# Performance work log

Measured on AMD Instinct MI355X. Metric: run time of the kernel, lower is better.

The kernel has to match this reference:

```python
import jax, jax.numpy as jnp
import numpy as np

H, W = 32, 56
CK, CV = 64, 512
N = 16 * H * W  # long + work memory fully populated: 16 frames of H*W entries
TOP_K = 30


def setup_inputs() -> dict:
    key = jax.random.key(0)
    k1, k2, k3, k4, k5 = jax.random.split(key, 5)
    return {
        "q_key": jax.random.normal(k1, (1, CK, H, W), dtype=jnp.float32),
        "q_selection": jax.random.uniform(k2, (1, CK, H, W), dtype=jnp.float32),
        "mem_key": jax.random.normal(k3, (1, CK, N), dtype=jnp.float32),
        "mem_shrinkage": jax.random.uniform(k4, (1, N, 1), dtype=jnp.float32),
        "mem_value": jax.random.normal(k5, (2, CV, N), dtype=jnp.float32),
    }


def reference(q_key, q_selection, mem_key, mem_shrinkage, mem_value):
    b, ck, h, w = q_key.shape
    hw = h * w
    qk = q_key.reshape(1, ck, hw)          # [1, CK, HW]
    qs = q_selection.reshape(1, ck, hw)    # [1, CK, HW]

    mk = jnp.swapaxes(mem_key, 1, 2)       # [1, N, CK]
    # negative weighted squared L2 distance via matmul algebra
    a_sq = jnp.matmul(mk * mk, qs)                    # [1, N, HW]
    two_ab = 2.0 * jnp.matmul(mk, qk * qs)            # [1, N, HW]
    b_sq = jnp.sum(qs * qk * qk, axis=1, keepdims=True)  # [1, 1, HW]
    sim = (-a_sq + two_ab - b_sq) * mem_shrinkage / jnp.sqrt(jnp.float32(ck))  # [1, N, HW]

    # topk over the memory axis (dim=1), softmax over selected entries, scatter back
    simT = jnp.swapaxes(sim, 1, 2)                    # [1, HW, N]
    vals, idx = jax.lax.top_k(simT, TOP_K)            # [1, HW, K]
    x_exp = jnp.exp(vals)
    x_exp = x_exp / jnp.sum(x_exp, axis=-1, keepdims=True)
    i0 = jnp.arange(1)[:, None, None]
    i1 = jnp.arange(hw)[None, :, None]
    affT = jnp.zeros_like(simT).at[i0, i1, idx].set(x_exp)  # [1, HW, N]
    affinity = jnp.swapaxes(affT, 1, 2)               # [1, N, HW]

    out = jnp.matmul(mem_value, affinity)             # [2, CV, HW] (batch-broadcast)
    return out.reshape(2, CV, h, w)
```

## Files before the change

### kernel.cpp

```cpp
#include <hip/hip_runtime.h>
#include <math.h>

#define HW      1792
#define NMEM    28672
#define NCHUNK  3584
#define TOPK    30
#define CTARGET 64
#define SCAP    80
#define SIMB    448
#define WPS     7

typedef __attribute__((ext_vector_type(8))) short bf16x8;
typedef __attribute__((ext_vector_type(8))) unsigned short u16x8;
typedef __attribute__((ext_vector_type(4))) float f32x4;
typedef __attribute__((ext_vector_type(4))) _Float16 h4;

static __device__ __forceinline__ unsigned short f2bf(float v) {
  unsigned b = __float_as_uint(v);
  return (unsigned short)((b + 0x7FFFu + ((b >> 16) & 1u)) >> 16);
}
static __device__ __forceinline__ float bf2f(unsigned short h) {
  return __uint_as_float(((unsigned)h) << 16);
}
static __device__ __forceinline__ unsigned fkey(float v) {
  return __float_as_uint(-v) & 0x7FFFFFFFu;
}
static __device__ __forceinline__ void gl_lds16(const void* g, void* l) {
  __builtin_amdgcn_global_load_lds(
      (const __attribute__((address_space(1))) unsigned*)g,
      (__attribute__((address_space(3))) unsigned*)l, 16, 0, 0);
}
#define WSYNC() do { asm volatile("s_waitcnt lgkmcnt(0)" ::: "memory"); \
                     __builtin_amdgcn_wave_barrier(); } while (0)

__global__ __launch_bounds__(256)
void k_prep_b(const float* __restrict__ mk, const float* __restrict__ shr_in,
              unsigned short* __restrict__ Bh,
              float* __restrict__ mkT, float* __restrict__ shr_s)
{
  const int n = blockIdx.x * 256 + threadIdx.x;
  shr_s[n] = shr_in[n] * 0.125f;
  for (int cb = 0; cb < 64; cb += 8) {
    u16x8 h1, h2;
    float vv[8];
    #pragma unroll
    for (int j = 0; j < 8; ++j) {
      float v = mk[(size_t)(cb + j) * NMEM + n];
      vv[j] = v;
      h1[j] = f2bf(v);
      h2[j] = f2bf(v * v);
    }
    const int s = cb >> 3;
    *reinterpret_cast<u16x8*>(&Bh[((size_t)s * NMEM + n) * 8])       = h1;
    *reinterpret_cast<u16x8*>(&Bh[((size_t)(s + 8) * NMEM + n) * 8]) = h2;
    *reinterpret_cast<float4*>(&mkT[(size_t)n * 64 + cb])     = make_float4(vv[0], vv[1], vv[2], vv[3]);
    *reinterpret_cast<float4*>(&mkT[(size_t)n * 64 + cb + 4]) = make_float4(vv[4], vv[5], vv[6], vv[7]);
  }
}

__global__ __launch_bounds__(256)
void k_prep_u(const float* __restrict__ q_key, const float* __restrict__ q_sel,
              unsigned short* __restrict__ Uh, unsigned short* __restrict__ Ul,
              float* __restrict__ bsq)
{
  const int p = blockIdx.x * 256 + threadIdx.x;
  float bs = 0.f;
  for (int cb = 0; cb < 64; cb += 8) {
    u16x8 h1, l1, h2, l2;
    #pragma unroll
    for (int j = 0; j < 8; ++j) {
      int c = cb + j;
      float k = q_key[(size_t)c * HW + p];
      float s = q_sel[(size_t)c * HW + p];
      float u = 2.f * k * s;
      float w = -s;
      bs = fmaf(s * k, k, bs);
      unsigned short h = f2bf(u); h1[j] = h; l1[j] = f2bf(u - bf2f(h));
      unsigned short g = f2bf(w); h2[j] = g; l2[j] = f2bf(w - bf2f(g));
    }
    const int s = cb >> 3;
    *reinterpret_cast<u16x8*>(&Uh[((size_t)s * HW + p) * 8])       = h1;
    *reinterpret_cast<u16x8*>(&Ul[((size_t)s * HW + p) * 8])       = l1;
    *reinterpret_cast<u16x8*>(&Uh[((size_t)(s + 8) * HW + p) * 8]) = h2;
    *reinterpret_cast<u16x8*>(&Ul[((size_t)(s + 8) * HW + p) * 8]) = l2;
  }
  bsq[p] = bs;
}

__global__ __launch_bounds__(256, 2)
void k_sim(const unsigned short* __restrict__ Uh, const unsigned short* __restrict__ Ul,
           const unsigned short* __restrict__ Bh,
           const float* __restrict__ bsq, const float* __restrict__ shr_s,
           float* __restrict__ pmax)
{
  __shared__ char smem[65536] __attribute__((aligned(16)));
  const int tid = threadIdx.x;
  const int wid = tid >> 6, lane = tid & 63;
  const int lr = lane & 15, lg = lane >> 4;
  const int pb = blockIdx.x % 14, st = blockIdx.x / 14;
  const int pw = pb * 128 + wid * 32;
  const int w0 = st * WPS;

  bf16x8 a0h[4], a0l[4], a1h[4], a1l[4];
  #pragma unroll
  for (int t = 0; t < 4; ++t) {
    const size_t e0 = ((size_t)(t * 4 + lg) * HW + pw + lr) * 8;
    const size_t e1 = e0 + 16 * 8;
    a0h[t] = *reinterpret_cast<const bf16x8*>(&Uh[e0]);
    a0l[t] = *reinterpret_cast<const bf16x8*>(&Ul[e0]);
    a1h[t] = *reinterpret_cast<const bf16x8*>(&Uh[e1]);
    a1l[t] = *reinterpret_cast<const bf16x8*>(&Ul[e1]);
  }
  float bq[2][4];
  #pragma unroll
  for (int pt = 0; pt < 2; ++pt)
    #pragma unroll
    for (int r = 0; r < 4; ++r) bq[pt][r] = bsq[pw + pt * 16 + 4 * lg + r];

  auto stage = [&](int buf, int i) {
    const int n0 = (w0 + i) * 128;
    #pragma unroll
    for (int j = 0; j < 8; ++j) {
      const int idx = j * 256 + tid;
      const int s = idx >> 7, rr = idx & 127;
      gl_lds16((const char*)Bh + ((size_t)s * NMEM + n0 + rr) * 16,
               smem + buf * 32768 + idx * 16);
    }
  };

  stage(0, 0);
  int buf = 0;
  for (int i = 0; i < WPS; ++i) {
    __syncthreads();
    if (i + 1 < WPS) stage(buf ^ 1, i + 1);

    f32x4 acc[2][8];
    #pragma unroll
    for (int a = 0; a < 2; ++a)
      #pragma unroll
      for (int b = 0; b < 8; ++b) acc[a][b] = (f32x4){0.f, 0.f, 0.f, 0.f};

    const short* lb = (const short*)(smem + buf * 32768);
    #pragma unroll
    for (int t = 0; t < 4; ++t) {
      #pragma unroll
      for (int nt = 0; nt < 8; ++nt) {
        bf16x8 bh = *reinterpret_cast<const bf16x8*>(
            &lb[((t * 4 + lg) * 128 + nt * 16 + lr) * 8]);
        acc[0][nt] = __builtin_amdgcn_mfma_f32_16x16x32_bf16(a0h[t], bh, acc[0][nt], 0, 0, 0);
        acc[0][nt] = __builtin_amdgcn_mfma_f32_16x16x32_bf16(a0l[t], bh, acc[0][nt], 0, 0, 0);
        acc[1][nt] = __builtin_amdgcn_mfma_f32_16x16x32_bf16(a1h[t], bh, acc[1][nt], 0, 0, 0);
        acc[1][nt] = __builtin_amdgcn_mfma_f32_16x16x32_bf16(a1l[t], bh, acc[1][nt], 0, 0, 0);
      }
    }

    const int wgl = w0 + i;
    const int n0 = wgl * 128;
    float shv[8];
    #pragma unroll
    for (int nt = 0; nt < 8; ++nt) shv[nt] = shr_s[n0 + nt * 16 + lr];
    #pragma unroll
    for (int pt = 0; pt < 2; ++pt) {
      #pragma unroll
      for (int r = 0; r < 4; ++r) {
        float mx = -INFINITY;
        #pragma unroll
        for (int nt = 0; nt < 8; ++nt)
          mx = fmaxf(mx, (acc[pt][nt][r] - bq[pt][r]) * shv[nt]);
        pmax[(size_t)(pw + pt * 16 + 4 * lg + r) * NCHUNK + wgl * 16 + lr] = mx;
      }
    }
    buf ^= 1;
  }
}

__device__ __forceinline__ void wave_cross(const int* h, int lane, int target,
                                           int& B, int& nA)
{
  int hv[16]; int ls = 0;
  #pragma unroll
  for (int k = 0; k < 16; ++k) { hv[k] = h[(k << 6) + lane]; ls += hv[k]; }
  int sc = ls;
  #pragma unroll
  for (int off = 1; off < 64; off <<= 1) {
    int t = __shfl_up(sc, off);
    if (lane >= off) sc += t;
  }
  int run = sc - ls;
  int myB = -1, mynA = 0;
  #pragma unroll
  for (int k = 0; k < 16; ++k) {
    if (run < target && run + hv[k] >= target) { myB = lane * 16 + k; mynA = run; }
    run += hv[k];
  }
  unsigned long long ball = __ballot(myB >= 0);
  int src = __ffsll((long long)ball) - 1;
  B = __shfl(myB, src); nA = __shfl(mynA, src);
}

__global__ __launch_bounds__(256, 2)
void k_select(const float* __restrict__ pmax, const float* __restrict__ mkT,
              const float* __restrict__ q_key, const float* __restrict__ q_sel,
              const float* __restrict__ shr_s,
              float* __restrict__ wgt, int* __restrict__ widx)
{
  __shared__ int                hist[4][1024];
  __shared__ unsigned long long pk[4][640];
  __shared__ short              slist[4][SCAP];
  __shared__ float              sqk[4][64], sqs[4][64];

  const int w = threadIdx.x >> 6, lane = threadIdx.x & 63;
  const int pix = blockIdx.x * 4 + w;
  int* h = hist[w];
  unsigned long long* p = pk[w];
  short* sl = slist[w];

  auto ph = [](int b) { return ((b & 15) << 6) | (b >> 4); };

  sqk[w][lane] = q_key[(size_t)lane * HW + pix];
  sqs[w][lane] = q_sel[(size_t)lane * HW + pix];

  float m[56];
  const float* pm = pmax + (size_t)pix * NCHUNK;
  #pragma unroll
  for (int j = 0; j < 56; ++j) m[j] = pm[lane + 64 * j];

  #pragma unroll
  for (int k = 0; k < 16; ++k) h[lane + 64 * k] = 0;
  WSYNC();
  #pragma unroll
  for (int j = 0; j < 56; ++j) atomicAdd(&h[ph(fkey(m[j]) >> 21)], 1);
  WSYNC();
  int B1, nA1;
  wave_cross(h, lane, CTARGET, B1, nA1);

  #pragma unroll
  for (int k = 0; k < 16; ++k) h[lane + 64 * k] = 0;
  WSYNC();
  #pragma unroll
  for (int j = 0; j < 56; ++j) {
    unsigned u = fkey(m[j]);
    if ((int)(u >> 21) == B1) atomicAdd(&h[ph((u >> 11) & 1023)], 1);
  }
  WSYNC();
  int Bs1, nAs1;
  wave_cross(h, lane, CTARGET - nA1, Bs1, nAs1);

  int nsurv = 0;
  #pragma unroll
  for (int j = 0; j < 56; ++j) {
    unsigned u = fkey(m[j]);
    int bin = (int)(u >> 21);
    bool keep = (bin < B1) || (bin == B1 && (int)((u >> 11) & 1023) <= Bs1);
    unsigned long long ball = __ballot(keep);
    if (keep) {
      int pos = nsurv + __popcll(ball & ((1ull << lane) - 1ull));
      if (pos < SCAP) sl[pos] = (short)(lane + 64 * j);
    }
    nsurv += __popcll(ball);
  }
  nsurv = (nsurv < SCAP) ? nsurv : SCAP;
  const int NC = nsurv * 8;

  #pragma unroll
  for (int t = 0; t < 10; ++t) p[lane + (t << 6)] = 0ull;
  WSYNC();
  const float4* k4p = reinterpret_cast<const float4*>(sqk[w]);
  const float4* s4p = reinterpret_cast<const float4*>(sqs[w]);
  for (int c = lane; c < NC; c += 64) {
    const int cc = sl[c >> 3];
    const int n = ((cc >> 4) << 7) + (cc & 15) + ((c & 7) << 4);
    const float4* mr = reinterpret_cast<const float4*>(mkT + (size_t)n * 64);
    float a0 = 0.f, a1 = 0.f, a2 = 0.f, a3 = 0.f;
    #pragma unroll
    for (int j = 0; j < 16; j += 4) {
      #pragma unroll
      for (int jj = 0; jj < 4; ++jj) {
        float4 q = mr[j + jj], kk = k4p[j + jj], ss = s4p[j + jj];
        float d0 = q.x - kk.x, d1 = q.y - kk.y, d2 = q.z - kk.z, d3 = q.w - kk.w;
        float pj = fmaf(ss.x * d0, d0,
                   fmaf(ss.y * d1, d1,
                   fmaf(ss.z * d2, d2, ss.w * d3 * d3)));
        if (jj == 0) a0 += pj; else if (jj == 1) a1 += pj;
        else if (jj == 2) a2 += pj; else a3 += pj;
      }
    }
    float v = -((a0 + a1) + (a2 + a3)) * shr_s[n];
    p[c] = ((unsigned long long)(0x7FFFFFFFu - fkey(v)) << 32) |
           (unsigned long long)(0xFFFFFFFFu - (unsigned)n);
  }
  WSYNC();

  unsigned long long bk = 0ull; int bp = -1;
  #pragma unroll
  for (int t = 0; t < 10; ++t) {
    unsigned long long v = p[lane + (t << 6)];
    if (v > bk) { bk = v; bp = lane + (t << 6); }
  }
  float esum = 0.f, myv = 0.f;
  int myn = 0;
  for (int r = 0; r < TOPK; ++r) {
    unsigned long long gk = bk; int gp = bp;
    #pragma unroll
    for (int off = 1; off < 64; off <<= 1) {
      unsigned long long ok = __shfl_xor(gk, off);
      int op = __shfl_xor(gp, off);
      if (ok > gk) { gk = ok; gp = op; }
    }
    float v = -__uint_as_float(0x7FFFFFFFu - (unsigned)(gk >> 32));
    int n = (int)(0xFFFFFFFFu - (unsigned)(gk & 0xFFFFFFFFu));
    esum += expf(v);
    if (lane == r) { myv = v; myn = n; }
    if (lane == (gp & 63)) {
      p[gp] = 0ull;
      asm volatile("s_waitcnt lgkmcnt(0)" ::: "memory");
      bk = 0ull; bp = -1;
      #pragma unroll
      for (int t = 0; t < 10; ++t) {
        unsigned long long vv = p[lane + (t << 6)];
        if (vv > bk) { bk = vv; bp = lane + (t << 6); }
      }
    }
  }
  if (lane < TOPK) {
    wgt [(size_t)pix * 32 + lane] = expf(myv) / esum;
    widx[(size_t)pix * 32 + lane] = myn;
  }
}

__global__ __launch_bounds__(256)
void k_transpose_h(const float* __restrict__ mv, _Float16* __restrict__ mvT)
{
  __shared__ float t[64][65];
  const int n0 = blockIdx.x * 64, ch0 = blockIdx.y * 64;
  const int tid = threadIdx.x;
  for (int i = tid; i < 64 * 16; i += 256) {
    int r = i >> 4, c4 = (i & 15) << 2;
    float4 v = *reinterpret_cast<const float4*>(&mv[(size_t)(ch0 + r) * NMEM + n0 + c4]);
    t[r][c4] = v.x; t[r][c4 + 1] = v.y; t[r][c4 + 2] = v.z; t[r][c4 + 3] = v.w;
  }
  __syncthreads();
  for (int i = tid; i < 64 * 16; i += 256) {
    int r = i >> 4, c4 = (i & 15) << 2;
    h4 hv = {(_Float16)t[c4][r], (_Float16)t[c4 + 1][r],
             (_Float16)t[c4 + 2][r], (_Float16)t[c4 + 3][r]};
    *reinterpret_cast<h4*>(&mvT[(size_t)(n0 + r) * 1024 + ch0 + c4]) = hv;
  }
}

__global__ __launch_bounds__(256)
void k_gather_h(const _Float16* __restrict__ mvT, const float* __restrict__ wgt,
                const int* __restrict__ widx, float* __restrict__ out)
{
  __shared__ float sw[8][TOPK];
  __shared__ int   si[8][TOPK];
  __shared__ float sbuf[256][9];
  const int p0 = blockIdx.x * 8, chg = blockIdx.y * 256;
  const int tid = threadIdx.x;

  for (int i = tid; i < 8 * TOPK; i += 256) {
    int q = i / TOPK, k = i - q * TOPK;
    sw[q][k] = wgt [(size_t)(p0 + q) * 32 + k];
    si[q][k] = widx[(size_t)(p0 + q) * 32 + k];
  }
  __syncthreads();

  const int ch = chg + tid;
  #pragma unroll 2
  for (int q = 0; q < 8; ++q) {
    float a = 0.f;
    #pragma unroll
    for (int k = 0; k < TOPK; ++k)
      a = fmaf(sw[q][k], (float)mvT[(size_t)si[q][k] * 1024 + ch], a);
    sbuf[tid][q] = a;
  }
  __syncthreads();

  for (int i = tid; i < 256 * 8; i += 256) {
    int cl = i >> 3, q = i & 7;
    out[(size_t)(chg + cl) * HW + p0 + q] = sbuf[cl][q];
  }
}

__global__ __launch_bounds__(256)
void k_gather_f(const float* __restrict__ src, const float* __restrict__ wgt,
                const int* __restrict__ widx, float* __restrict__ out,
                long n_stride, long ch_stride)
{
  __shared__ float sw[8][TOPK];
  __shared__ int   si[8][TOPK];
  __shared__ float sbuf[256][9];
  const int p0 = blockIdx.x * 8, chg = blockIdx.y * 256;
  const int tid = threadIdx.x;

  for (int i = tid; i < 8 * TOPK; i += 256) {
    int q = i / TOPK, k = i - q * TOPK;
    sw[q][k] = wgt [(size_t)(p0 + q) * 32 + k];
    si[q][k] = widx[(size_t)(p0 + q) * 32 + k];
  }
  __syncthreads();

  const int ch = chg + tid;
  #pragma unroll 2
  for (int q = 0; q < 8; ++q) {
    float a = 0.f;
    #pragma unroll
    for (int k = 0; k < TOPK; ++k)
      a = fmaf(sw[q][k], src[(size_t)si[q][k] * n_stride + (size_t)ch * ch_stride], a);
    sbuf[tid][q] = a;
  }
  __syncthreads();

  for (int i = tid; i < 256 * 8; i += 256) {
    int cl = i >> 3, q = i & 7;
    out[(size_t)(chg + cl) * HW + p0 + q] = sbuf[cl][q];
  }
}

extern "C" void kernel_launch(void* const* d_in, const int* in_sizes, int n_in,
                              void* d_out, int out_size, void* d_ws, size_t ws_size,
                              hipStream_t stream)
{
  (void)in_sizes; (void)n_in; (void)out_size;
  const float* q_key     = (const float*)d_in[0];
  const float* q_sel     = (const float*)d_in[1];
  const float* mem_key   = (const float*)d_in[2];
  const float* mem_shr   = (const float*)d_in[3];
  const float* mem_value = (const float*)d_in[4];
  float* out = (float*)d_out;

  char* ws = (char*)d_ws;
  size_t off = 0;
  auto alloc = [&](size_t b) { size_t c = off; off = (off + b + 255) & ~(size_t)255; return c; };
  size_t o_w   = alloc((size_t)HW * 32 * 4);
  size_t o_wi  = alloc((size_t)HW * 32 * 4);
  size_t o_pr  = off;
  size_t o_bh  = alloc((size_t)NMEM * 128 * 2);
  size_t o_uh  = alloc((size_t)HW * 128 * 2);
  size_t o_ul  = alloc((size_t)HW * 128 * 2);
  size_t o_bsq = alloc((size_t)HW * 4);
  size_t o_shr = alloc((size_t)NMEM * 4);
  size_t o_mkT = alloc((size_t)NMEM * 64 * 4);
  size_t o_pm  = alloc((size_t)HW * NCHUNK * 4);
  size_t o_end = off;

  float*          wg   = (float*)(ws + o_w);
  int*            wi   = (int*)  (ws + o_wi);
  unsigned short* Bh   = (unsigned short*)(ws + o_bh);
  unsigned short* Uh   = (unsigned short*)(ws + o_uh);
  unsigned short* Ul   = (unsigned short*)(ws + o_ul);
  float*          bsq  = (float*)(ws + o_bsq);
  float*          shr  = (float*)(ws + o_shr);
  float*          mkT  = (float*)(ws + o_mkT);
  float*          pmx  = (float*)(ws + o_pm);

  const size_t mvh_sz = (size_t)NMEM * 1024 * 2;

  k_prep_b<<<NMEM / 256, 256, 0, stream>>>(mem_key, mem_shr, Bh, mkT, shr);
  k_prep_u<<<HW / 256, 256, 0, stream>>>(q_key, q_sel, Uh, Ul, bsq);
  k_sim<<<SIMB, 256, 0, stream>>>(Uh, Ul, Bh, bsq, shr, pmx);
  k_select<<<HW / 4, 256, 0, stream>>>(pmx, mkT, q_key, q_sel, shr, wg, wi);

  if (ws_size >= o_end + mvh_sz) {
    _Float16* mvT = (_Float16*)(ws + o_end);
    k_transpose_h<<<dim3(NMEM / 64, 16), 256, 0, stream>>>(mem_value, mvT);
    k_gather_h<<<dim3(HW / 8, 4), 256, 0, stream>>>(mvT, wg, wi, out);
  } else if (ws_size >= o_pr + mvh_sz) {
    _Float16* mvT = (_Float16*)(ws + o_pr);
    k_transpose_h<<<dim3(NMEM / 64, 16), 256, 0, stream>>>(mem_value, mvT);
    k_gather_h<<<dim3(HW / 8, 4), 256, 0, stream>>>(mvT, wg, wi, out);
  } else {
    k_gather_f<<<dim3(HW / 8, 4), 256, 0, stream>>>(
        mem_value, wg, wi, out, 1, NMEM);
  }
}
```

Measured before the change: 169.7 us.

## Fuse value transpose into top-k select kernel and replace serial top-k with radix select

Merges the mem_value fp16 transpose into the select kernel as extra interleaved blocks, so the memory-bound transpose overlaps the latency-bound selection instead of running as a separate launch. The 30-round serial argmax over candidates is replaced by a second two-level radix histogram pass plus a rank-by-shuffle sort of at most 64 finalists. Histograms shrink to 512 bins, candidate caps are lowered (CTARGET 48, SCAP 64), and occupancy is raised to 4 blocks per CU. The lower caps could drop true top-k entries when many values tie near the cutoff.

```diff
diff --git a/kernel.cpp b/kernel.cpp
--- a/kernel.cpp
+++ b/kernel.cpp
@@ -5,15 +5,18 @@
 #define NMEM    28672
 #define NCHUNK  3584
 #define TOPK    30
-#define CTARGET 64
-#define SCAP    80
+#define CTARGET 48
+#define SCAP    64
+#define FINCAP  64
 #define SIMB    448
 #define WPS     7
+#define NSELB   448
 
 typedef __attribute__((ext_vector_type(8))) short bf16x8;
 typedef __attribute__((ext_vector_type(8))) unsigned short u16x8;
 typedef __attribute__((ext_vector_type(4))) float f32x4;
 typedef __attribute__((ext_vector_type(4))) _Float16 h4;
+typedef unsigned long long ull;
 
 static __device__ __forceinline__ unsigned short f2bf(float v) {
   unsigned b = __float_as_uint(v);
@@ -174,12 +177,23 @@
   }
 }
 
-__device__ __forceinline__ void wave_cross(const int* h, int lane, int target,
-                                           int& B, int& nA)
-{
-  int hv[16]; int ls = 0;
-  #pragma unroll
-  for (int k = 0; k < 16; ++k) { hv[k] = h[(k << 6) + lane]; ls += hv[k]; }
+struct SelS {
+  int   hist[4][512];
+  ull   pk[4][512];
+  ull   fin[4][FINCAP];
+  short sl[4][SCAP];
+  float sqk[4][64], sqs[4][64];
+};
+union SMemU { SelS sel; float tt[64][65]; };
+
+static __device__ __forceinline__ int ph(int b) { return ((b & 7) << 6) | (b >> 3); }
+
+static __device__ __forceinline__ void wave_cross8(const int* h, int lane, int target,
+                                                   int& B, int& nA)
+{
+  int hv[8]; int ls = 0;
+  #pragma unroll
+  for (int k = 0; k < 8; ++k) { hv[k] = h[(k << 6) + lane]; ls += hv[k]; }
   int sc = ls;
   #pragma unroll
   for (int off = 1; off < 64; off <<= 1) {
@@ -189,36 +203,60 @@
   int run = sc - ls;
   int myB = -1, mynA = 0;
   #pragma unroll
-  for (int k = 0; k < 16; ++k) {
-    if (run < target && run + hv[k] >= target) { myB = lane * 16 + k; mynA = run; }
+  for (int k = 0; k < 8; ++k) {
+    if (run < target && run + hv[k] >= target) { myB = lane * 8 + k; mynA = run; }
     run += hv[k];
   }
-  unsigned long long ball = __ballot(myB >= 0);
+  ull ball = __ballot(myB >= 0);
   int src = __ffsll((long long)ball) - 1;
   B = __shfl(myB, src); nA = __shfl(mynA, src);
 }
 
-__global__ __launch_bounds__(256, 2)
-void k_select(const float* __restrict__ pmax, const float* __restrict__ mkT,
-              const float* __restrict__ q_key, const float* __restrict__ q_sel,
-              const float* __restrict__ shr_s,
-              float* __restrict__ wgt, int* __restrict__ widx)
-{
-  __shared__ int                hist[4][1024];
-  __shared__ unsigned long long pk[4][640];
-  __shared__ short              slist[4][SCAP];
-  __shared__ float              sqk[4][64], sqs[4][64];
-
-  const int w = threadIdx.x >> 6, lane = threadIdx.x & 63;
-  const int pix = blockIdx.x * 4 + w;
-  int* h = hist[w];
-  unsigned long long* p = pk[w];
-  short* sl = slist[w];
-
-  auto ph = [](int b) { return ((b & 15) << 6) | (b >> 4); };
-
-  sqk[w][lane] = q_key[(size_t)lane * HW + pix];
-  sqs[w][lane] = q_sel[(size_t)lane * HW + pix];
+__global__ __launch_bounds__(256, 4)
+void k_selT(const float* __restrict__ pmax, const float* __restrict__ mkT,
+            const float* __restrict__ q_key, const float* __restrict__ q_sel,
+            const float* __restrict__ shr_s,
+            float* __restrict__ wgt, int* __restrict__ widx,
+            const float* __restrict__ mv, _Float16* __restrict__ mvT)
+{
+  __shared__ SMemU sm;
+  const int tid = threadIdx.x;
+
+  int sg = -1, tb = -1;
+  if (gridDim.x > NSELB) {
+    const int g = blockIdx.x / 17, r = blockIdx.x % 17;
+    if (r == 0) sg = g; else tb = g * 16 + (r - 1);
+  } else {
+    sg = blockIdx.x;
+  }
+
+  if (tb >= 0) {
+    const int n0 = (tb % 448) * 64, ch0 = (tb / 448) * 64;
+    for (int i = tid; i < 64 * 16; i += 256) {
+      int r = i >> 4, c4 = (i & 15) << 2;
+      float4 v = *reinterpret_cast<const float4*>(&mv[(size_t)(ch0 + r) * NMEM + n0 + c4]);
+      sm.tt[r][c4] = v.x; sm.tt[r][c4 + 1] = v.y;
+      sm.tt[r][c4 + 2] = v.z; sm.tt[r][c4 + 3] = v.w;
+    }
+    __syncthreads();
+    for (int i = tid; i < 64 * 16; i += 256) {
+      int r = i >> 4, c4 = (i & 15) << 2;
+      h4 hv = {(_Float16)sm.tt[c4][r], (_Float16)sm.tt[c4 + 1][r],
+               (_Float16)sm.tt[c4 + 2][r], (_Float16)sm.tt[c4 + 3][r]};
+      *reinterpret_cast<h4*>(&mvT[(size_t)(n0 + r) * 1024 + ch0 + c4]) = hv;
+    }
+    return;
+  }
+
+  const int w = tid >> 6, lane = tid & 63;
+  const int pix = sg * 4 + w;
+  int*   h  = sm.sel.hist[w];
+  ull*   p  = sm.sel.pk[w];
+  ull*   fin = sm.sel.fin[w];
+  short* sl = sm.sel.sl[w];
+
+  sm.sel.sqk[w][lane] = q_key[(size_t)lane * HW + pix];
+  sm.sel.sqs[w][lane] = q_sel[(size_t)lane * HW + pix];
 
   float m[56];
   const float* pm = pmax + (size_t)pix * NCHUNK;
@@ -226,33 +264,33 @@
   for (int j = 0; j < 56; ++j) m[j] = pm[lane + 64 * j];
 
   #pragma unroll
-  for (int k = 0; k < 16; ++k) h[lane + 64 * k] = 0;
-  WSYNC();
-  #pragma unroll
-  for (int j = 0; j < 56; ++j) atomicAdd(&h[ph(fkey(m[j]) >> 21)], 1);
+  for (int k = 0; k < 8; ++k) h[lane + 64 * k] = 0;
+  WSYNC();
+  #pragma unroll
+  for (int j = 0; j < 56; ++j) atomicAdd(&h[ph(fkey(m[j]) >> 22)], 1);
   WSYNC();
   int B1, nA1;
-  wave_cross(h, lane, CTARGET, B1, nA1);
-
-  #pragma unroll
-  for (int k = 0; k < 16; ++k) h[lane + 64 * k] = 0;
+  wave_cross8(h, lane, CTARGET, B1, nA1);
+
+  #pragma unroll
+  for (int k = 0; k < 8; ++k) h[lane + 64 * k] = 0;
   WSYNC();
   #pragma unroll
   for (int j = 0; j < 56; ++j) {
     unsigned u = fkey(m[j]);
-    if ((int)(u >> 21) == B1) atomicAdd(&h[ph((u >> 11) & 1023)], 1);
+    if ((int)(u >> 22) == B1) atomicAdd(&h[ph((u >> 13) & 511)], 1);
   }
   WSYNC();
   int Bs1, nAs1;
-  wave_cross(h, lane, CTARGET - nA1, Bs1, nAs1);
+  wave_cross8(h, lane, CTARGET - nA1, Bs1, nAs1);
 
   int nsurv = 0;
   #pragma unroll
   for (int j = 0; j < 56; ++j) {
     unsigned u = fkey(m[j]);
-    int bin = (int)(u >> 21);
-    bool keep = (bin < B1) || (bin == B1 && (int)((u >> 11) & 1023) <= Bs1);
-    unsigned long long ball = __ballot(keep);
+    int b1 = (int)(u >> 22);
+    bool keep = (b1 < B1) || (b1 == B1 && (int)((u >> 13) & 511) <= Bs1);
+    ull ball = __ballot(keep);
     if (keep) {
       int pos = nsurv + __popcll(ball & ((1ull << lane) - 1ull));
       if (pos < SCAP) sl[pos] = (short)(lane + 64 * j);
@@ -261,70 +299,102 @@
   }
   nsurv = (nsurv < SCAP) ? nsurv : SCAP;
   const int NC = nsurv * 8;
-
-  #pragma unroll
-  for (int t = 0; t < 10; ++t) p[lane + (t << 6)] = 0ull;
-  WSYNC();
-  const float4* k4p = reinterpret_cast<const float4*>(sqk[w]);
-  const float4* s4p = reinterpret_cast<const float4*>(sqs[w]);
+  WSYNC();
+
+  const float4* k4p = reinterpret_cast<const float4*>(sm.sel.sqk[w]);
+  const float4* s4p = reinterpret_cast<const float4*>(sm.sel.sqs[w]);
   for (int c = lane; c < NC; c += 64) {
     const int cc = sl[c >> 3];
     const int n = ((cc >> 4) << 7) + (cc & 15) + ((c & 7) << 4);
     const float4* mr = reinterpret_cast<const float4*>(mkT + (size_t)n * 64);
-    float a0 = 0.f, a1 = 0.f, a2 = 0.f, a3 = 0.f;
-    #pragma unroll
-    for (int j = 0; j < 16; j += 4) {
-      #pragma unroll
-      for (int jj = 0; jj < 4; ++jj) {
-        float4 q = mr[j + jj], kk = k4p[j + jj], ss = s4p[j + jj];
-        float d0 = q.x - kk.x, d1 = q.y - kk.y, d2 = q.z - kk.z, d3 = q.w - kk.w;
-        float pj = fmaf(ss.x * d0, d0,
-                   fmaf(ss.y * d1, d1,
-                   fmaf(ss.z * d2, d2, ss.w * d3 * d3)));
-        if (jj == 0) a0 += pj; else if (jj == 1) a1 += pj;
-        else if (jj == 2) a2 += pj; else a3 += pj;
-      }
-    }
-    float v = -((a0 + a1) + (a2 + a3)) * shr_s[n];
-    p[c] = ((unsigned long long)(0x7FFFFFFFu - fkey(v)) << 32) |
-           (unsigned long long)(0xFFFFFFFFu - (unsigned)n);
-  }
-  WSYNC();
-
-  unsigned long long bk = 0ull; int bp = -1;
-  #pragma unroll
-  for (int t = 0; t < 10; ++t) {
-    unsigned long long v = p[lane + (t << 6)];
-    if (v > bk) { bk = v; bp = lane + (t << 6); }
-  }
-  float esum = 0.f, myv = 0.f;
-  int myn = 0;
-  for (int r = 0; r < TOPK; ++r) {
-    unsigned long long gk = bk; int gp = bp;
-    #pragma unroll
-    for (int off = 1; off < 64; off <<= 1) {
-      unsigned long long ok = __shfl_xor(gk, off);
-      int op = __shfl_xor(gp, off);
-      if (ok > gk) { gk = ok; gp = op; }
-    }
-    float v = -__uint_as_float(0x7FFFFFFFu - (unsigned)(gk >> 32));
-    int n = (int)(0xFFFFFFFFu - (unsigned)(gk & 0xFFFFFFFFu));
-    esum += expf(v);
-    if (lane == r) { myv = v; myn = n; }
-    if (lane == (gp & 63)) {
-      p[gp] = 0ull;
-      asm volatile("s_waitcnt lgkmcnt(0)" ::: "memory");
-      bk = 0ull; bp = -1;
-      #pragma unroll
-      for (int t = 0; t < 10; ++t) {
-        unsigned long long vv = p[lane + (t << 6)];
-        if (vv > bk) { bk = vv; bp = lane + (t << 6); }
-      }
-    }
-  }
-  if (lane < TOPK) {
-    wgt [(size_t)pix * 32 + lane] = expf(myv) / esum;
-    widx[(size_t)pix * 32 + lane] = myn;
+    float s0 = 0.f, s1 = 0.f, s2 = 0.f, s3 = 0.f;
+    #pragma unroll
+    for (int j = 0; j < 4; ++j) {
+      float4 q0 = mr[4 * j], q1 = mr[4 * j + 1], q2 = mr[4 * j + 2], q3 = mr[4 * j + 3];
+      float4 a0 = k4p[4 * j], a1 = k4p[4 * j + 1], a2 = k4p[4 * j + 2], a3 = k4p[4 * j + 3];
+      float4 b0 = s4p[4 * j], b1 = s4p[4 * j + 1], b2 = s4p[4 * j + 2], b3 = s4p[4 * j + 3];
+      float d;
+      d = q0.x - a0.x; s0 = fmaf(b0.x * d, d, s0);
+      d = q0.y - a0.y; s1 = fmaf(b0.y * d, d, s1);
+      d = q0.z - a0.z; s2 = fmaf(b0.z * d, d, s2);
+      d = q0.w - a0.w; s3 = fmaf(b0.w * d, d, s3);
+      d = q1.x - a1.x; s0 = fmaf(b1.x * d, d, s0);
+      d = q1.y - a1.y; s1 = fmaf(b1.y * d, d, s1);
+      d = q1.z - a1.z; s2 = fmaf(b1.z * d, d, s2);
+      d = q1.w - a1.w; s3 = fmaf(b1.w * d, d, s3);
+      d = q2.x - a2.x; s0 = fmaf(b2.x * d, d, s0);
+      d = q2.y - a2.y; s1 = fmaf(b2.y * d, d, s1);
+      d = q2.z - a2.z; s2 = fmaf(b2.z * d, d, s2);
+      d = q2.w - a2.w; s3 = fmaf(b2.w * d, d, s3);
+      d = q3.x - a3.x; s0 = fmaf(b3.x * d, d, s0);
+      d = q3.y - a3.y; s1 = fmaf(b3.y * d, d, s1);
+      d = q3.z - a3.z; s2 = fmaf(b3.z * d, d, s2);
+      d = q3.w - a3.w; s3 = fmaf(b3.w * d, d, s3);
+    }
+    float v = -((s0 + s1) + (s2 + s3)) * shr_s[n];
+    p[c] = ((ull)(0x7FFFFFFFu - fkey(v)) << 32) |
+           (ull)(0xFFFFFFFFu - (unsigned)n);
+  }
+  WSYNC();
+
+  #pragma unroll
+  for (int k = 0; k < 8; ++k) h[lane + 64 * k] = 0;
+  WSYNC();
+  for (int c = lane; c < NC; c += 64) {
+    unsigned qk = 0x7FFFFFFFu - (unsigned)(p[c] >> 32);
+    atomicAdd(&h[ph(qk >> 22)], 1);
+  }
+  WSYNC();
+  int B2, nA2;
+  wave_cross8(h, lane, TOPK, B2, nA2);
+
+  #pragma unroll
+  for (int k = 0; k < 8; ++k) h[lane + 64 * k] = 0;
+  WSYNC();
+  for (int c = lane; c < NC; c += 64) {
+    unsigned qk = 0x7FFFFFFFu - (unsigned)(p[c] >> 32);
+    if ((int)(qk >> 22) == B2) atomicAdd(&h[ph((qk >> 13) & 511)], 1);
+  }
+  WSYNC();
+  int Bs2, nAs2;
+  wave_cross8(h, lane, TOPK - nA2, Bs2, nAs2);
+
+  int nfin = 0;
+  for (int c0 = 0; c0 < NC; c0 += 64) {
+    int c = c0 + lane;
+    bool isf = false; ull key = 0ull;
+    if (c < NC) {
+      key = p[c];
+      unsigned qk = 0x7FFFFFFFu - (unsigned)(key >> 32);
+      int b1 = (int)(qk >> 22);
+      isf = (b1 < B2) || (b1 == B2 && (int)((qk >> 13) & 511) <= Bs2);
+    }
+    ull ball = __ballot(isf);
+    if (isf) {
+      int pos = nfin + __popcll(ball & ((1ull << lane) - 1ull));
+      if (pos < FINCAP) fin[pos] = key;
+    }
+    nfin += __popcll(ball);
+  }
+  WSYNC();
+  const int nf = (nfin < FINCAP) ? nfin : FINCAP;
+
+  ull myk = (lane < nf) ? fin[lane] : 0ull;
+  int r = 0;
+  #pragma unroll
+  for (int sft = 1; sft < 64; ++sft) {
+    ull ok = __shfl_xor(myk, sft);
+    r += (ok > myk) ? 1 : 0;
+  }
+  float v = -__uint_as_float(0x7FFFFFFFu - (unsigned)(myk >> 32));
+  bool sel = (lane < nf) && (r < TOPK);
+  float e = sel ? expf(v) : 0.f;
+  float es = e;
+  #pragma unroll
+  for (int off = 32; off > 0; off >>= 1) es += __shfl_xor(es, off);
+  if (sel) {
+    wgt [(size_t)pix * 32 + r] = e / es;
+    widx[(size_t)pix * 32 + r] = (int)(0xFFFFFFFFu - (unsigned)(myk & 0xFFFFFFFFu));
   }
 }
 
@@ -459,17 +529,21 @@
   k_prep_b<<<NMEM / 256, 256, 0, stream>>>(mem_key, mem_shr, Bh, mkT, shr);
   k_prep_u<<<HW / 256, 256, 0, stream>>>(q_key, q_sel, Uh, Ul, bsq);
   k_sim<<<SIMB, 256, 0, stream>>>(Uh, Ul, Bh, bsq, shr, pmx);
-  k_select<<<HW / 4, 256, 0, stream>>>(pmx, mkT, q_key, q_sel, shr, wg, wi);
 
   if (ws_size >= o_end + mvh_sz) {
     _Float16* mvT = (_Float16*)(ws + o_end);
-    k_transpose_h<<<dim3(NMEM / 64, 16), 256, 0, stream>>>(mem_value, mvT);
+    k_selT<<<NSELB * 17, 256, 0, stream>>>(pmx, mkT, q_key, q_sel, shr,
+                                           wg, wi, mem_value, mvT);
     k_gather_h<<<dim3(HW / 8, 4), 256, 0, stream>>>(mvT, wg, wi, out);
   } else if (ws_size >= o_pr + mvh_sz) {
+    k_selT<<<NSELB, 256, 0, stream>>>(pmx, mkT, q_key, q_sel, shr,
+                                      wg, wi, mem_value, nullptr);
     _Float16* mvT = (_Float16*)(ws + o_pr);
     k_transpose_h<<<dim3(NMEM / 64, 16), 256, 0, stream>>>(mem_value, mvT);
     k_gather_h<<<dim3(HW / 8, 4), 256, 0, stream>>>(mvT, wg, wi, out);
   } else {
+    k_selT<<<NSELB, 256, 0, stream>>>(pmx, mkT, q_key, q_sel, shr,
+                                      wg, wi, mem_value, nullptr);
     k_gather_f<<<dim3(HW / 8, 4), 256, 0, stream>>>(
         mem_value, wg, wi, out, 1, NMEM);
   }
```

After: 155.8 us. 8.2% less time.
